# Optimization experiments

Hardware: AMD Instinct MI355X
Metric: run time of the kernel (lower is better)

The kernel has to match this reference:

```python
import jax, jax.numpy as jnp
import numpy as np

N_EMBD = 1024
N_HEAD = 16
B, T = 2, 2048
EPS_LN = 1e-5
EPS_RENORM = 1e-8


def _layernorm(x, w, b):
    mu = jnp.mean(x, axis=-1, keepdims=True)
    var = jnp.mean(jnp.square(x - mu), axis=-1, keepdims=True)
    return (x - mu) * jax.lax.rsqrt(var + EPS_LN) * w + b


def setup_inputs() -> dict:
    key = jax.random.key(0)
    ks = jax.random.split(key, 8)
    C = N_EMBD
    s = 0.02
    return {
        "x": jax.random.normal(ks[0], (B, T, C), jnp.float32),
        "ln1_w": jnp.ones((C,), jnp.float32),
        "ln1_b": jnp.zeros((C,), jnp.float32),
        "w_attn": jax.random.normal(ks[1], (C, 3 * C), jnp.float32) * s,
        "b_attn": jnp.zeros((3 * C,), jnp.float32),
        "w_attn_proj": jax.random.normal(ks[2], (C, C), jnp.float32) * s,
        "b_attn_proj": jnp.zeros((C,), jnp.float32),
        "threshold": jnp.full((N_HEAD,), 0.01, jnp.float32),
        "leak": jnp.full((N_HEAD,), 2.0, jnp.float32),
        "steepness": jnp.full((N_HEAD,), 2.0, jnp.float32),
        "ln2_w": jnp.ones((C,), jnp.float32),
        "ln2_b": jnp.zeros((C,), jnp.float32),
        "w_fc": jax.random.normal(ks[3], (C, 4 * C), jnp.float32) * s,
        "b_fc": jnp.zeros((4 * C,), jnp.float32),
        "w_mlp_proj": jax.random.normal(ks[4], (4 * C, C), jnp.float32) * s,
        "b_mlp_proj": jnp.zeros((C,), jnp.float32),
    }


def _ember_block(x, ln1_w, ln1_b, w_attn, b_attn, w_attn_proj, b_attn_proj,
                 threshold, leak, steepness, ln2_w, ln2_b,
                 w_fc, b_fc, w_mlp_proj, b_mlp_proj):
    Bx, Tx, C = x.shape
    H = N_HEAD
    D = C // H

    h = _layernorm(x, ln1_w, ln1_b)
    qkv = h @ w_attn + b_attn                      # [B,T,3C]
    q, k, v = jnp.split(qkv, 3, axis=-1)
    q = q.reshape(Bx, Tx, H, D).transpose(0, 2, 1, 3)  # [B,H,T,D]
    k = k.reshape(Bx, Tx, H, D).transpose(0, 2, 1, 3)
    v = v.reshape(Bx, Tx, H, D).transpose(0, 2, 1, 3)

    att = jnp.einsum('bhqd,bhkd->bhqk', q, k) * (1.0 / np.sqrt(D))
    causal = jnp.tril(jnp.ones((Tx, Tx), bool))
    att = jnp.where(causal[None, None], att, -jnp.inf)
    p = jax.nn.softmax(att, axis=-1)               # [B,H,T,T]

    # per-head LIF gating
    th = (jnp.abs(threshold) * 0.1)[None, :, None, None]
    lk = jax.nn.sigmoid(leak)[None, :, None, None]
    st = jax.nn.softplus(steepness)[None, :, None, None]
    fire = jax.nn.sigmoid(st * (p - th))
    w = fire + lk * (1.0 - fire)
    m = p * w
    m = m / (jnp.sum(m, axis=-1, keepdims=True) + EPS_RENORM)

    y = jnp.einsum('bhqk,bhkd->bhqd', m, v)
    y = y.transpose(0, 2, 1, 3).reshape(Bx, Tx, C)
    y = y @ w_attn_proj + b_attn_proj
    x = x + y

    h2 = _layernorm(x, ln2_w, ln2_b)
    h2 = jax.nn.gelu(h2 @ w_fc + b_fc, approximate=False)
    x = x + (h2 @ w_mlp_proj + b_mlp_proj)
    return x


def reference(x, ln1_w, ln1_b, w_attn, b_attn, w_attn_proj, b_attn_proj,
              threshold, leak, steepness, ln2_w, ln2_b,
              w_fc, b_fc, w_mlp_proj, b_mlp_proj):
    return _ember_block(x, ln1_w, ln1_b, w_attn, b_attn, w_attn_proj, b_attn_proj,
                        threshold, leak, steepness, ln2_w, ln2_b,
                        w_fc, b_fc, w_mlp_proj, b_mlp_proj)
```

## Files before the change

### kernel.cpp

```cpp
#include <hip/hip_runtime.h>
#include <hip/hip_bf16.h>
#include <math.h>

typedef __bf16 bf16_t;
typedef __bf16 bf16x8 __attribute__((ext_vector_type(8)));
typedef __bf16 bf16x4 __attribute__((ext_vector_type(4)));
typedef float  f32x4  __attribute__((ext_vector_type(4)));
typedef unsigned int u32;

static constexpr int C_    = 1024;
static constexpr int NH    = 16;
static constexpr int DH    = 64;
static constexpr int BB    = 2;
static constexpr int TT    = 2048;
static constexpr int MROWS = BB * TT;
static constexpr float LOG2E = 1.4426950408889634f;

__device__ __forceinline__ void gload_lds16(const bf16_t* src, bf16_t* dst) {
  __builtin_amdgcn_global_load_lds(
      (const __attribute__((address_space(1))) u32*)(src),
      (__attribute__((address_space(3))) u32*)(dst),
      16, 0, 0);
}

__device__ __forceinline__ u32 cvt_pk_bf16(float a, float b) {
  u32 r;
  asm("v_cvt_pk_bf16_f32 %0, %1, %2" : "=v"(r) : "v"(a), "v"(b));
  return r;
}

__device__ __forceinline__ float fexp2(float x) {
#if __has_builtin(__builtin_amdgcn_exp2f)
  return __builtin_amdgcn_exp2f(x);
#else
  return exp2f(x);
#endif
}
__device__ __forceinline__ float frcp(float x) {
#if __has_builtin(__builtin_amdgcn_rcpf)
  return __builtin_amdgcn_rcpf(x);
#else
  return 1.0f / x;
#endif
}

__device__ __forceinline__ int sc_to_t(int s, int c) {
  if (s < 32)  return s;
  if (s < 64)  return 32 + (s - 32) * 2 + c;
  if (s < 96)  return 96 + (s - 64) * 3 + c;
  return 192 + (s - 96) * 4 + c;
}

__device__ __forceinline__ void item64_to_uc(int item, int& u, int& c) {
  if (item < 8)       { u = item;               c = 0; }
  else if (item < 24) { int v = item - 8;  u = 8  + (v >> 1); c = v & 1; }
  else if (item < 48) { int v = item - 24; u = 16 + v / 3;    c = v - 3 * (v / 3); }
  else                { int v = item - 48; u = 24 + (v >> 2); c = v & 3; }
}

__global__ __launch_bounds__(256) void ln_bf16(
    const float* __restrict__ x, const float* __restrict__ w,
    const float* __restrict__ b, bf16_t* __restrict__ out)
{
  const int row = blockIdx.x;
  const int tid = threadIdx.x;
  const float4 v = reinterpret_cast<const float4*>(x + (size_t)row * C_)[tid];
  float s  = v.x + v.y + v.z + v.w;
  float s2 = v.x*v.x + v.y*v.y + v.z*v.z + v.w*v.w;
#pragma unroll
  for (int m = 1; m < 64; m <<= 1) { s += __shfl_xor(s, m); s2 += __shfl_xor(s2, m); }
  __shared__ float red[8];
  const int wv = tid >> 6;
  if ((tid & 63) == 0) { red[wv] = s; red[4 + wv] = s2; }
  __syncthreads();
  s  = red[0] + red[1] + red[2] + red[3];
  s2 = red[4] + red[5] + red[6] + red[7];
  const float mu   = s * (1.0f / C_);
  const float rstd = rsqrtf(s2 * (1.0f / C_) - mu * mu + 1e-5f);
  const float4 wv4 = reinterpret_cast<const float4*>(w)[tid];
  const float4 bv4 = reinterpret_cast<const float4*>(b)[tid];
  bf16x4 o;
  o[0] = (bf16_t)((v.x - mu) * rstd * wv4.x + bv4.x);
  o[1] = (bf16_t)((v.y - mu) * rstd * wv4.y + bv4.y);
  o[2] = (bf16_t)((v.z - mu) * rstd * wv4.z + bv4.z);
  o[3] = (bf16_t)((v.w - mu) * rstd * wv4.w + bv4.w);
  *reinterpret_cast<bf16x4*>(out + (size_t)row * C_ + tid * 4) = o;
}

__global__ __launch_bounds__(256) void ln2_fuse(
    const float* __restrict__ p0, const bf16_t* __restrict__ p1,
    const float* __restrict__ xin, const float* __restrict__ pbias,
    const float* __restrict__ w, const float* __restrict__ b,
    float* __restrict__ x2out, bf16_t* __restrict__ out)
{
  const int row = blockIdx.x;
  const int tid = threadIdx.x;
  const size_t base = (size_t)row * C_ + tid * 4;
  const float4 v0 = *reinterpret_cast<const float4*>(p0 + base);
  const bf16x4 v1 = *reinterpret_cast<const bf16x4*>(p1 + base);
  const float4 xr = *reinterpret_cast<const float4*>(xin + base);
  const float4 pb = *reinterpret_cast<const float4*>(pbias + tid * 4);
  float4 v;
  v.x = v0.x + (float)v1[0] + pb.x + xr.x;
  v.y = v0.y + (float)v1[1] + pb.y + xr.y;
  v.z = v0.z + (float)v1[2] + pb.z + xr.z;
  v.w = v0.w + (float)v1[3] + pb.w + xr.w;
  *reinterpret_cast<float4*>(x2out + base) = v;

  float s  = v.x + v.y + v.z + v.w;
  float s2 = v.x*v.x + v.y*v.y + v.z*v.z + v.w*v.w;
#pragma unroll
  for (int m = 1; m < 64; m <<= 1) { s += __shfl_xor(s, m); s2 += __shfl_xor(s2, m); }
  __shared__ float red[8];
  const int wv = tid >> 6;
  if ((tid & 63) == 0) { red[wv] = s; red[4 + wv] = s2; }
  __syncthreads();
  s  = red[0] + red[1] + red[2] + red[3];
  s2 = red[4] + red[5] + red[6] + red[7];
  const float mu   = s * (1.0f / C_);
  const float rstd = rsqrtf(s2 * (1.0f / C_) - mu * mu + 1e-5f);
  const float4 wv4 = reinterpret_cast<const float4*>(w)[tid];
  const float4 bv4 = reinterpret_cast<const float4*>(b)[tid];
  bf16x4 o;
  o[0] = (bf16_t)((v.x - mu) * rstd * wv4.x + bv4.x);
  o[1] = (bf16_t)((v.y - mu) * rstd * wv4.y + bv4.y);
  o[2] = (bf16_t)((v.z - mu) * rstd * wv4.z + bv4.z);
  o[3] = (bf16_t)((v.w - mu) * rstd * wv4.w + bv4.w);
  *reinterpret_cast<bf16x4*>(out + base) = o;
}

__global__ __launch_bounds__(256) void combine3(
    float* __restrict__ out, const bf16_t* __restrict__ p1,
    const bf16_t* __restrict__ p2, const bf16_t* __restrict__ p3,
    const float* __restrict__ bias, const float* __restrict__ resid)
{
  const size_t idx = ((size_t)blockIdx.x * 256 + threadIdx.x) * 4;
  float4 o = *reinterpret_cast<const float4*>(out + idx);
  const bf16x4 a = *reinterpret_cast<const bf16x4*>(p1 + idx);
  const bf16x4 b = *reinterpret_cast<const bf16x4*>(p2 + idx);
  const bf16x4 c = *reinterpret_cast<const bf16x4*>(p3 + idx);
  const float4 r = *reinterpret_cast<const float4*>(resid + idx);
  const int col = (int)(idx & (C_ - 1));
  const float4 bv = *reinterpret_cast<const float4*>(bias + col);
  o.x += (float)a[0] + (float)b[0] + (float)c[0] + bv.x + r.x;
  o.y += (float)a[1] + (float)b[1] + (float)c[1] + bv.y + r.y;
  o.z += (float)a[2] + (float)b[2] + (float)c[2] + bv.z + r.z;
  o.w += (float)a[3] + (float)b[3] + (float)c[3] + bv.w + r.w;
  *reinterpret_cast<float4*>(out + idx) = o;
}

__global__ __launch_bounds__(256) void transpose_w(
    const float* __restrict__ in, bf16_t* __restrict__ out, int K, int N)
{
  __shared__ float tile[32][33];
  const int tx = threadIdx.x & 31, ty = threadIdx.x >> 5;
  const int n0 = blockIdx.x * 32, k0 = blockIdx.y * 32;
#pragma unroll
  for (int i = 0; i < 4; ++i)
    tile[ty + i * 8][tx] = in[(size_t)(k0 + ty + i * 8) * N + n0 + tx];
  __syncthreads();
#pragma unroll
  for (int i = 0; i < 4; ++i)
    out[(size_t)(n0 + ty + i * 8) * K + k0 + tx] = (bf16_t)tile[tx][ty + i * 8];
}

__global__ __launch_bounds__(256) void transpose_v(
    const bf16_t* __restrict__ in, bf16_t* __restrict__ out)
{
  __shared__ bf16_t tile[32][33];
  const int bh = blockIdx.z;
  const bf16_t* src = in  + (size_t)bh * TT * DH;
  bf16_t*       dst = out + (size_t)bh * TT * DH;
  const int tx = threadIdx.x & 31, ty = threadIdx.x >> 5;
  const int t0 = blockIdx.x * 32, d0 = blockIdx.y * 32;
#pragma unroll
  for (int i = 0; i < 4; ++i)
    tile[ty + i * 8][tx] = src[(size_t)(t0 + ty + i * 8) * DH + d0 + tx];
  __syncthreads();
#pragma unroll
  for (int i = 0; i < 4; ++i)
    dst[(size_t)(d0 + ty + i * 8) * TT + t0 + tx] = tile[tx][ty + i * 8];
}

template<int EPI>
__global__ __launch_bounds__(256) void gemm_bf16(
    const bf16_t* __restrict__ A, const bf16_t* __restrict__ Bt,
    const float* __restrict__ bias, const float* __restrict__ resid,
    float* __restrict__ fout, bf16_t* __restrict__ bout0,
    bf16_t* __restrict__ bout1, bf16_t* __restrict__ bout2,
    int M, int N, int Kc, int Kfull)
{
  constexpr int BM = 128, BN = 128, BK = 64;
  __shared__ bf16_t As[BM * BK];
  __shared__ bf16_t Bs[BN * BK];
  const int tid  = threadIdx.x;
  const int wave = tid >> 6, lane = tid & 63;
  const int r = lane & 15, g = lane >> 4;
  const int wm = wave >> 1, wn = wave & 1;
  const int bm = blockIdx.x, bn = blockIdx.y;
  const int z  = blockIdx.z;
  const int kstart = z * Kc;

  const bf16_t* Abase = A  + (size_t)bm * BM * Kfull;
  const bf16_t* Bbase = Bt + (size_t)bn * BN * Kfull;

  f32x4 acc[4][4] = {};

  for (int kt = kstart; kt < kstart + Kc; kt += BK) {
#pragma unroll
    for (int it = 0; it < 4; ++it) {
      const int c0 = it * 256 + wave * 64;
      const int idx = c0 + lane;
      const int rr = idx >> 3, cc = idx & 7;
      const int gs = cc ^ (rr & 7);
      gload_lds16(Abase + (size_t)rr * Kfull + kt + gs * 8, As + c0 * 8);
    }
#pragma unroll
    for (int it = 0; it < 4; ++it) {
      const int c0 = it * 256 + wave * 64;
      const int idx = c0 + lane;
      const int rr = idx >> 3, cc = idx & 7;
      const int gs = cc ^ (rr & 7);
      gload_lds16(Bbase + (size_t)rr * Kfull + kt + gs * 8, Bs + c0 * 8);
    }
    asm volatile("s_waitcnt vmcnt(0)" ::: "memory");
    __syncthreads();
#pragma unroll
    for (int s = 0; s < 2; ++s) {
      bf16x8 af[4], bfr[4];
#pragma unroll
      for (int mi = 0; mi < 4; ++mi) {
        const int rr = wm * 64 + mi * 16 + r;
        const int ch = (s * 4 + g) ^ (rr & 7);
        af[mi] = *reinterpret_cast<const bf16x8*>(&As[rr * BK + ch * 8]);
      }
#pragma unroll
      for (int ni = 0; ni < 4; ++ni) {
        const int rr = wn * 64 + ni * 16 + r;
        const int ch = (s * 4 + g) ^ (rr & 7);
        bfr[ni] = *reinterpret_cast<const bf16x8*>(&Bs[rr * BK + ch * 8]);
      }
#pragma unroll
      for (int mi = 0; mi < 4; ++mi)
#pragma unroll
        for (int ni = 0; ni < 4; ++ni)
          acc[mi][ni] = __builtin_amdgcn_mfma_f32_16x16x32_bf16(
              af[mi], bfr[ni], acc[mi][ni], 0, 0, 0);
    }
    __syncthreads();
  }

#pragma unroll
  for (int mi = 0; mi < 4; ++mi) {
#pragma unroll
    for (int ni = 0; ni < 4; ++ni) {
      const int grow0 = bm * BM + wm * 64 + mi * 16 + g * 4;
      const int gcol  = bn * BN + wn * 64 + ni * 16 + r;
      const float bv = (EPI == 3) ? 0.f : bias[gcol];
#pragma unroll
      for (int i = 0; i < 4; ++i) {
        const int grow = grow0 + i;
        float v = acc[mi][ni][i] + bv;
        if constexpr (EPI == 0) {
          const int which = gcol >> 10;
          const int c0 = gcol & 1023;
          const int hh = c0 >> 6, dd = c0 & 63;
          const int bb = grow >> 11, t = grow & 2047;
          bf16_t* dst = (which == 0) ? bout0 : (which == 1) ? bout1 : bout2;
          dst[((size_t)(bb * NH + hh) * TT + t) * DH + dd] = (bf16_t)v;
        } else if constexpr (EPI == 1) {
          const size_t o = (size_t)grow * N + gcol;
          fout[o] = v + resid[o];
        } else if constexpr (EPI == 2) {
          const float gl = 0.5f * v * (1.0f + erff(v * 0.70710678118654752f));
          bout0[(size_t)grow * N + gcol] = (bf16_t)gl;
        } else {
          const size_t o = (size_t)grow * N + gcol;
          if (z == 0) fout[o] = v;
          else {
            bf16_t* pb = (z == 1) ? bout0 : (z == 2) ? bout1 : bout2;
            pb[o] = (bf16_t)v;
          }
        }
      }
    }
  }
}


__global__ __launch_bounds__(256, 4) void attn_p1(
    const bf16_t* __restrict__ Q, const bf16_t* __restrict__ Km,
    float2* __restrict__ mzP)
{
  __shared__ bf16_t Ks[2][64 * 64];
  const int tid = threadIdx.x;
  const int w = tid >> 6, lane = tid & 63;
  const int r = lane & 15, g = lane >> 4;
  const int bid = blockIdx.x;
  const int bh  = (bid & 7) * 4 + ((bid >> 3) & 3);
  int u, c; item64_to_uc(bid >> 5, u, c);
  const int cmax = u >> 3;
  const bool diag = (c == cmax);
  const int nt = diag ? (u & 7) + 1 : 8;
  const int s = 4 * u + w;
  const int row0 = u * 64 + w * 16;
  const int qrow = row0 + r;

  const bf16_t* Qh = Q  + (size_t)bh * TT * DH;
  const bf16_t* Kh = Km + (size_t)bh * TT * DH;
  const float SCL = 0.125f * LOG2E;

  bf16x8 qf[2];
#pragma unroll
  for (int s2 = 0; s2 < 2; ++s2) {
    bf16x8 t = *reinterpret_cast<const bf16x8*>(Qh + (size_t)qrow * DH + s2 * 32 + g * 8);
#pragma unroll
    for (int i = 0; i < 8; ++i) t[i] = (bf16_t)((float)t[i] * SCL);
    qf[s2] = t;
  }

  auto STAGEK = [&](int b, int t8) {
#pragma unroll
    for (int it = 0; it < 2; ++it) {
      const int idx = it * 256 + tid;
      const int rr = idx >> 3, cc = idx & 7, gs = cc ^ (rr & 7);
      gload_lds16(Kh + (size_t)(c * 512 + t8 * 64 + rr) * DH + gs * 8, &Ks[b][idx * 8]);
    }
  };

  float runM = -1e30f, runZ = 0.f;
  STAGEK(0, 0);
  for (int t8 = 0; t8 < nt; ++t8) {
    const int b = t8 & 1;
    asm volatile("s_waitcnt vmcnt(0)" ::: "memory");
    __syncthreads();
    if (t8 + 1 < nt) STAGEK(b ^ 1, t8 + 1);
    f32x4 sfT[4] = {};
#pragma unroll
    for (int s2 = 0; s2 < 2; ++s2) {
      bf16x8 kf[4];
#pragma unroll
      for (int ni = 0; ni < 4; ++ni)
        kf[ni] = *reinterpret_cast<const bf16x8*>(
            &Ks[b][(ni * 16 + r) * 64 + (((s2 << 2) | g) ^ (r & 7)) * 8]);
#pragma unroll
      for (int ni = 0; ni < 4; ++ni)
        sfT[ni] = __builtin_amdgcn_mfma_f32_16x16x32_bf16(kf[ni], qf[s2], sfT[ni], 0, 0, 0);
    }
    const bool dm = diag && (t8 == nt - 1);
    const int kbase = c * 512 + t8 * 64;
    float xv[16];
#pragma unroll
    for (int ni = 0; ni < 4; ++ni)
#pragma unroll
      for (int j = 0; j < 4; ++j) {
        float x = sfT[ni][j];
        if (dm) {
          const int kcol = kbase + ni * 16 + g * 4 + j;
          if (kcol > qrow) x = -1e30f;
        }
        xv[ni * 4 + j] = x;
      }
    float nm = runM;
#pragma unroll
    for (int e = 0; e < 16; ++e) nm = fmaxf(nm, xv[e]);
    float z = runZ * fexp2(runM - nm);
#pragma unroll
    for (int e = 0; e < 16; ++e) z += fexp2(xv[e] - nm);
    runM = nm; runZ = z;
  }
#pragma unroll
  for (int msk = 16; msk < 64; msk <<= 1) {
    const float om = __shfl_xor(runM, msk), oz = __shfl_xor(runZ, msk);
    const float nm = fmaxf(runM, om);
    runZ = runZ * fexp2(runM - nm) + oz * fexp2(om - nm);
    runM = nm;
  }
  if (lane < 16)
    mzP[((size_t)(bh * 128 + s) * 4 + c) * 16 + r] = make_float2(runM, runZ);
}

__global__ __launch_bounds__(256, 4) void attn_p3(
    const bf16_t* __restrict__ Q, const bf16_t* __restrict__ Km,
    const bf16_t* __restrict__ Vt, const float2* __restrict__ mzP,
    bf16_t* __restrict__ Y, uint2* __restrict__ yaccA,
    uint2* __restrict__ yaccB, float* __restrict__ denP,
    const float* __restrict__ thrp, const float* __restrict__ leakp,
    const float* __restrict__ steepp)
{
  __shared__ bf16_t Ks[2][64 * 64];
  __shared__ bf16_t Vs[2][64 * 64];
  __shared__ __align__(16) u32 Ms[4][512];

  const int tid = threadIdx.x;
  const int w = tid >> 6, lane = tid & 63;
  const int r = lane & 15, g = lane >> 4;
  const int bid = blockIdx.x;
  const int bh  = (bid & 7) * 4 + ((bid >> 3) & 3);
  int u, c; item64_to_uc(bid >> 5, u, c);
  const int cmax = u >> 3;
  const bool diag = (c == cmax);
  const int nt = diag ? (u & 7) + 1 : 8;
  const int nch = cmax + 1;
  const int s = 4 * u + w;
  const int row0 = u * 64 + w * 16;
  const int qrow = row0 + r;
  const int hh = bh & (NH - 1), bb = bh >> 4;

  const bf16_t* Qh  = Q  + (size_t)bh * TT * DH;
  const bf16_t* Kh  = Km + (size_t)bh * TT * DH;
  const bf16_t* Vth = Vt + (size_t)bh * TT * DH;

  const float lk  = 1.0f / (1.0f + expf(-leakp[hh]));
  const float ilk = 1.0f - lk;
  const float st  = log1pf(expf(steepp[hh]));
  const float Lst = LOG2E * st;
  const float A0  = Lst * (fabsf(thrp[hh]) * 0.1f);

  float M = -1e30f, Z = 0.f;
  for (int c2 = 0; c2 < nch; ++c2) {
    const float2 mz = mzP[((size_t)(bh * 128 + s) * 4 + c2) * 16 + r];
    const float nm = fmaxf(M, mz.x);
    Z = Z * fexp2(M - nm) + mz.y * fexp2(mz.x - nm);
    M = nm;
  }
  const float rcpZ = frcp(Z);

  const float SCL = 0.125f * LOG2E;
  bf16x8 qf[2];
#pragma unroll
  for (int s2 = 0; s2 < 2; ++s2) {
    bf16x8 t = *reinterpret_cast<const bf16x8*>(Qh + (size_t)qrow * DH + s2 * 32 + g * 8);
#pragma unroll
    for (int i = 0; i < 8; ++i) t[i] = (bf16_t)((float)t[i] * SCL);
    qf[s2] = t;
  }
  bf16x8 ones;
#pragma unroll
  for (int i = 0; i < 8; ++i) ones[i] = (bf16_t)1.0f;

  uint2* MsU2 = reinterpret_cast<uint2*>(&Ms[w][0]);
  uint4* MsU4 = reinterpret_cast<uint4*>(&Ms[w][0]);

  auto STAGE = [&](int b, int t8) {
    const int kbase = c * 512 + t8 * 64;
#pragma unroll
    for (int it = 0; it < 2; ++it) {
      const int idx = it * 256 + tid;
      const int rr = idx >> 3, cc = idx & 7, gs = cc ^ (rr & 7);
      gload_lds16(Kh + (size_t)(kbase + rr) * DH + gs * 8, &Ks[b][idx * 8]);
      gload_lds16(Vth + (size_t)rr * TT + kbase + gs * 8, &Vs[b][idx * 8]);
    }
  };

  f32x4 yacc[4] = {};
  f32x4 dacc = {};

  STAGE(0, 0);
  for (int t8 = 0; t8 < nt; ++t8) {
    const int b = t8 & 1;
    asm volatile("s_waitcnt vmcnt(0)" ::: "memory");
    __syncthreads();
    if (t8 + 1 < nt) STAGE(b ^ 1, t8 + 1);
    const int kbase = c * 512 + t8 * 64;
    f32x4 sfT[4] = {};
#pragma unroll
    for (int s2 = 0; s2 < 2; ++s2) {
      bf16x8 kf[4];
#pragma unroll
      for (int ni = 0; ni < 4; ++ni)
        kf[ni] = *reinterpret_cast<const bf16x8*>(
            &Ks[b][(ni * 16 + r) * 64 + (((s2 << 2) | g) ^ (r & 7)) * 8]);
#pragma unroll
      for (int ni = 0; ni < 4; ++ni)
        sfT[ni] = __builtin_amdgcn_mfma_f32_16x16x32_bf16(kf[ni], qf[s2], sfT[ni], 0, 0, 0);
    }
    const bool dm = diag && (t8 == nt - 1);
#pragma unroll
    for (int ni = 0; ni < 4; ++ni) {
      float mv[4];
#pragma unroll
      for (int j = 0; j < 4; ++j) {
        float x = sfT[ni][j];
        if (dm) {
          const int kcol = kbase + ni * 16 + g * 4 + j;
          if (kcol > qrow) x = -1e30f;
        }
        const float p    = fexp2(x - M) * rcpZ;
        const float fire = frcp(1.0f + fexp2(A0 - Lst * p));
        mv[j] = p * fmaf(ilk, fire, lk);
      }
      MsU2[r * 16 + ((4 * ni + g) ^ ((r & 7) << 1))] =
          make_uint2(cvt_pk_bf16(mv[0], mv[1]), cvt_pk_bf16(mv[2], mv[3]));
    }
#pragma unroll
    for (int s2 = 0; s2 < 2; ++s2) {
      const uint4 aw = MsU4[r * 8 + ((s2 * 4 + g) ^ (r & 7))];
      const bf16x8 af = __builtin_bit_cast(bf16x8, aw);
      bf16x8 vf[4];
#pragma unroll
      for (int ni = 0; ni < 4; ++ni)
        vf[ni] = *reinterpret_cast<const bf16x8*>(
            &Vs[b][(ni * 16 + r) * 64 + (((s2 << 2) | g) ^ (r & 7)) * 8]);
#pragma unroll
      for (int ni = 0; ni < 4; ++ni)
        yacc[ni] = __builtin_amdgcn_mfma_f32_16x16x32_bf16(af, vf[ni], yacc[ni], 0, 0, 0);
      dacc = __builtin_amdgcn_mfma_f32_16x16x32_bf16(af, ones, dacc, 0, 0, 0);
    }
  }

  if (nch == 1) {
#pragma unroll
    for (int j = 0; j < 4; ++j) {
      const float rd = frcp(dacc[j] + 1e-8f);
      const int t = row0 + g * 4 + j;
#pragma unroll
      for (int ni = 0; ni < 4; ++ni)
        Y[((size_t)(bb * TT + t)) * C_ + hh * DH + ni * 16 + r] =
            (bf16_t)(yacc[ni][j] * rd);
    }
  } else {
    const int pid = bh * 288 + (sc_to_t(s, c) - 32);
    uint2* pb = (pid < 4096) ? (yaccA + (size_t)pid * 256)
                             : (yaccB + (size_t)(pid - 4096) * 256);
#pragma unroll
    for (int ni = 0; ni < 4; ++ni)
      pb[ni * 64 + lane] =
          make_uint2(cvt_pk_bf16(yacc[ni][0], yacc[ni][1]),
                     cvt_pk_bf16(yacc[ni][2], yacc[ni][3]));
    if (r == 0)
      *reinterpret_cast<float4*>(&denP[(size_t)pid * 16 + g * 4]) =
          make_float4(dacc[0], dacc[1], dacc[2], dacc[3]);
  }
}

__global__ __launch_bounds__(256) void attn_p4(
    const uint2* __restrict__ yaccA, const uint2* __restrict__ yaccB,
    const float* __restrict__ denP, bf16_t* __restrict__ Y)
{
  const int bid = blockIdx.x;
  const int bh  = bid / 96;
  const int s   = 32 + (bid - bh * 96);
  const int nch = (s >> 5) + 1;
  const int hh = bh & (NH - 1), bb = bh >> 4;

  const int tid = threadIdx.x;
  const int w = tid >> 6, lane = tid & 63;
  const int r = lane & 15, g = lane >> 4;

  float acc[4] = {};
  float den[4] = {};
  for (int c = 0; c < nch; ++c) {
    const int pid = bh * 288 + (sc_to_t(s, c) - 32);
    const uint2* pb = (pid < 4096) ? (yaccA + (size_t)pid * 256)
                                   : (yaccB + (size_t)(pid - 4096) * 256);
    const uint2 u = pb[w * 64 + lane];
    acc[0] += __builtin_bit_cast(float, (u.x & 0xFFFFu) << 16);
    acc[1] += __builtin_bit_cast(float, (u.x & 0xFFFF0000u));
    acc[2] += __builtin_bit_cast(float, (u.y & 0xFFFFu) << 16);
    acc[3] += __builtin_bit_cast(float, (u.y & 0xFFFF0000u));
    const float4 d4 = *reinterpret_cast<const float4*>(&denP[(size_t)pid * 16 + g * 4]);
    den[0] += d4.x; den[1] += d4.y; den[2] += d4.z; den[3] += d4.w;
  }
#pragma unroll
  for (int j = 0; j < 4; ++j) {
    const float rd = 1.0f / (den[j] + 1e-8f);
    const int t = s * 16 + g * 4 + j;
    Y[((size_t)(bb * TT + t)) * C_ + hh * DH + w * 16 + r] = (bf16_t)(acc[j] * rd);
  }
}

extern "C" void kernel_launch(void* const* d_in, const int* in_sizes, int n_in,
                              void* d_out, int out_size, void* d_ws, size_t ws_size,
                              hipStream_t stream)
{
  const float* x      = (const float*)d_in[0];
  const float* ln1_w  = (const float*)d_in[1];
  const float* ln1_b  = (const float*)d_in[2];
  const float* w_attn = (const float*)d_in[3];
  const float* b_attn = (const float*)d_in[4];
  const float* w_proj = (const float*)d_in[5];
  const float* b_proj = (const float*)d_in[6];
  const float* thr    = (const float*)d_in[7];
  const float* leak   = (const float*)d_in[8];
  const float* steep  = (const float*)d_in[9];
  const float* ln2_w  = (const float*)d_in[10];
  const float* ln2_b  = (const float*)d_in[11];
  const float* w_fc   = (const float*)d_in[12];
  const float* b_fc   = (const float*)d_in[13];
  const float* w_mlp  = (const float*)d_in[14];
  const float* b_mlp  = (const float*)d_in[15];

  char* ws = (char*)d_ws;
  bf16_t* q    = (bf16_t*)(ws + 0);
  bf16_t* k    = (bf16_t*)(ws + 8388608);
  bf16_t* v    = (bf16_t*)(ws + 16777216);
  bf16_t* vT   = (bf16_t*)(ws + 25165824);
  bf16_t* gbuf = (bf16_t*)(ws + 0);
  bf16_t* hbuf = (bf16_t*)(ws + 33554432);
  float*  x2   = (float*) (ws + 41943040);
  bf16_t* wT_attn = (bf16_t*)(ws + 58720256);
  bf16_t* wT_proj = (bf16_t*)(ws + 65011712);
  bf16_t* wT_fc   = (bf16_t*)(ws + 67108864);
  bf16_t* wT_mlp  = (bf16_t*)(ws + 75497472);

  uint2* yaccA = (uint2*)(ws + 16777216);
  uint2* yaccB = (uint2*)(ws + 41943040);
  float* denP  = (float*)(ws + 52428800);
  float2* mzP  = (float2*)(ws + 53477376);

  bf16_t* pp1 = (bf16_t*)(ws + 0);
  bf16_t* mp1 = (bf16_t*)(ws + 33554432);
  bf16_t* mp2 = (bf16_t*)(ws + 58720256);
  bf16_t* mp3 = (bf16_t*)(ws + 67108864);

  float* out = (float*)d_out;

  ln_bf16<<<dim3(MROWS), dim3(256), 0, stream>>>(x, ln1_w, ln1_b, hbuf);
  transpose_w<<<dim3(96, 32),  dim3(256), 0, stream>>>(w_attn, wT_attn, 1024, 3072);
  transpose_w<<<dim3(32, 32),  dim3(256), 0, stream>>>(w_proj, wT_proj, 1024, 1024);
  transpose_w<<<dim3(128, 32), dim3(256), 0, stream>>>(w_fc,   wT_fc,   1024, 4096);
  transpose_w<<<dim3(32, 128), dim3(256), 0, stream>>>(w_mlp,  wT_mlp,  4096, 1024);

  gemm_bf16<0><<<dim3(32, 24, 1), dim3(256), 0, stream>>>(
      hbuf, wT_attn, b_attn, nullptr, nullptr, q, k, v, MROWS, 3072, 1024, 1024);
  transpose_v<<<dim3(64, 2, 32), dim3(256), 0, stream>>>(v, vT);

  attn_p1<<<dim3(2560), dim3(256), 0, stream>>>(q, k, mzP);
  attn_p3<<<dim3(2560), dim3(256), 0, stream>>>(
      q, k, vT, mzP, hbuf, yaccA, yaccB, denP, thr, leak, steep);
  attn_p4<<<dim3(3072), dim3(256), 0, stream>>>(yaccA, yaccB, denP, hbuf);

  gemm_bf16<3><<<dim3(32, 8, 2), dim3(256), 0, stream>>>(
      hbuf, wT_proj, nullptr, nullptr, x2, pp1, nullptr, nullptr,
      MROWS, 1024, 512, 1024);

  ln2_fuse<<<dim3(MROWS), dim3(256), 0, stream>>>(
      x2, pp1, x, b_proj, ln2_w, ln2_b, x2, hbuf);

  gemm_bf16<2><<<dim3(32, 32, 1), dim3(256), 0, stream>>>(
      hbuf, wT_fc, b_fc, nullptr, nullptr, gbuf, nullptr, nullptr,
      MROWS, 4096, 1024, 1024);

  gemm_bf16<3><<<dim3(32, 8, 4), dim3(256), 0, stream>>>(
      gbuf, wT_mlp, nullptr, nullptr, out, mp1, mp2, mp3,
      MROWS, 1024, 1024, 4096);

  combine3<<<dim3(4096), dim3(256), 0, stream>>>(out, mp1, mp2, mp3, b_mlp, x2);
}
```

Baseline: 295.2 us.

## Add double-buffered 256x256 tile GEMM for QKV and FC projections

Introduces a new GEMM kernel with 256x256 output tiles, 512 threads, XOR-swizzled LDS, double-buffered async global-to-LDS loads, grid swizzling and MFMA priority hints. It is used for the QKV projection and the FC+GELU GEMM. The old generic GEMM keeps only its split-K epilogue. Larger tiles raise arithmetic intensity and let loads overlap compute, but they launch far fewer blocks (192 and 256) on a chip with many CUs, which risks under-occupancy.

```diff
diff --git a/kernel.cpp b/kernel.cpp
--- a/kernel.cpp
+++ b/kernel.cpp
@@ -183,6 +183,106 @@
 }
 
 template<int EPI>
+__global__ __launch_bounds__(512, 2) void gemm256(
+    const bf16_t* __restrict__ A, const bf16_t* __restrict__ Bt,
+    const float* __restrict__ bias, bf16_t* __restrict__ bout0,
+    bf16_t* __restrict__ bout1, bf16_t* __restrict__ bout2,
+    int N, int K, int nbn)
+{
+  __shared__ bf16_t As[2][256 * 64];
+  __shared__ bf16_t Bs[2][256 * 64];
+  const int tid  = threadIdx.x;
+  const int wave = tid >> 6, lane = tid & 63;
+  const int r = lane & 15, g = lane >> 4;
+  const int wm = wave >> 2, wn = wave & 3;
+
+  const int cpx = gridDim.x >> 3;
+  const int swz = (blockIdx.x & 7) * cpx + (blockIdx.x >> 3);
+  const int bm = swz / nbn, bn = swz - bm * nbn;
+
+  const bf16_t* Abase = A  + (size_t)bm * 256 * K;
+  const bf16_t* Bbase = Bt + (size_t)bn * 256 * K;
+
+  f32x4 acc[8][4] = {};
+
+  auto STAGE = [&](int b, int kt) {
+#pragma unroll
+    for (int it = 0; it < 4; ++it) {
+      const int idx = it * 512 + tid;
+      const int rr = idx >> 3, cc = idx & 7, gs = cc ^ (rr & 7);
+      gload_lds16(Abase + (size_t)rr * K + kt + gs * 8, &As[b][idx * 8]);
+      gload_lds16(Bbase + (size_t)rr * K + kt + gs * 8, &Bs[b][idx * 8]);
+    }
+  };
+
+  const int NT = K >> 6;
+  STAGE(0, 0);
+  for (int t = 0; t < NT; ++t) {
+    const int b = t & 1;
+    if (t + 1 < NT) {
+      STAGE(b ^ 1, (t + 1) << 6);
+      asm volatile("s_waitcnt vmcnt(8)" ::: "memory");
+    } else {
+      asm volatile("s_waitcnt vmcnt(0)" ::: "memory");
+    }
+    __builtin_amdgcn_s_barrier();
+    asm volatile("" ::: "memory");
+#pragma unroll
+    for (int s2 = 0; s2 < 2; ++s2) {
+      bf16x8 af[8], bfr[4];
+#pragma unroll
+      for (int mi = 0; mi < 8; ++mi) {
+        const int rr = wm * 128 + mi * 16 + r;
+        const int ch = (s2 * 4 + g) ^ (rr & 7);
+        af[mi] = *reinterpret_cast<const bf16x8*>(&As[b][rr * 64 + ch * 8]);
+      }
+#pragma unroll
+      for (int ni = 0; ni < 4; ++ni) {
+        const int rr = wn * 64 + ni * 16 + r;
+        const int ch = (s2 * 4 + g) ^ (rr & 7);
+        bfr[ni] = *reinterpret_cast<const bf16x8*>(&Bs[b][rr * 64 + ch * 8]);
+      }
+      __builtin_amdgcn_s_setprio(1);
+#pragma unroll
+      for (int mi = 0; mi < 8; ++mi)
+#pragma unroll
+        for (int ni = 0; ni < 4; ++ni)
+          acc[mi][ni] = __builtin_amdgcn_mfma_f32_16x16x32_bf16(
+              af[mi], bfr[ni], acc[mi][ni], 0, 0, 0);
+      __builtin_amdgcn_s_setprio(0);
+    }
+    asm volatile("" ::: "memory");
+    __builtin_amdgcn_s_barrier();
+  }
+
+#pragma unroll
+  for (int mi = 0; mi < 8; ++mi) {
+#pragma unroll
+    for (int ni = 0; ni < 4; ++ni) {
+      const int grow0 = bm * 256 + wm * 128 + mi * 16 + g * 4;
+      const int gcol  = bn * 256 + wn * 64 + ni * 16 + r;
+      const float bv = bias[gcol];
+#pragma unroll
+      for (int i = 0; i < 4; ++i) {
+        const int grow = grow0 + i;
+        const float v = acc[mi][ni][i] + bv;
+        if constexpr (EPI == 0) {
+          const int which = gcol >> 10;
+          const int c0 = gcol & 1023;
+          const int hh = c0 >> 6, dd = c0 & 63;
+          const int bb = grow >> 11, tt = grow & 2047;
+          bf16_t* dst = (which == 0) ? bout0 : (which == 1) ? bout1 : bout2;
+          dst[((size_t)(bb * NH + hh) * TT + tt) * DH + dd] = (bf16_t)v;
+        } else {
+          const float gl = 0.5f * v * (1.0f + erff(v * 0.70710678118654752f));
+          bout0[(size_t)grow * N + gcol] = (bf16_t)gl;
+        }
+      }
+    }
+  }
+}
+
+template<int EPI>
 __global__ __launch_bounds__(256) void gemm_bf16(
     const bf16_t* __restrict__ A, const bf16_t* __restrict__ Bt,
     const float* __restrict__ bias, const float* __restrict__ resid,
@@ -256,31 +356,15 @@
     for (int ni = 0; ni < 4; ++ni) {
       const int grow0 = bm * BM + wm * 64 + mi * 16 + g * 4;
       const int gcol  = bn * BN + wn * 64 + ni * 16 + r;
-      const float bv = (EPI == 3) ? 0.f : bias[gcol];
 #pragma unroll
       for (int i = 0; i < 4; ++i) {
         const int grow = grow0 + i;
-        float v = acc[mi][ni][i] + bv;
-        if constexpr (EPI == 0) {
-          const int which = gcol >> 10;
-          const int c0 = gcol & 1023;
-          const int hh = c0 >> 6, dd = c0 & 63;
-          const int bb = grow >> 11, t = grow & 2047;
-          bf16_t* dst = (which == 0) ? bout0 : (which == 1) ? bout1 : bout2;
-          dst[((size_t)(bb * NH + hh) * TT + t) * DH + dd] = (bf16_t)v;
-        } else if constexpr (EPI == 1) {
-          const size_t o = (size_t)grow * N + gcol;
-          fout[o] = v + resid[o];
-        } else if constexpr (EPI == 2) {
-          const float gl = 0.5f * v * (1.0f + erff(v * 0.70710678118654752f));
-          bout0[(size_t)grow * N + gcol] = (bf16_t)gl;
-        } else {
-          const size_t o = (size_t)grow * N + gcol;
-          if (z == 0) fout[o] = v;
-          else {
-            bf16_t* pb = (z == 1) ? bout0 : (z == 2) ? bout1 : bout2;
-            pb[o] = (bf16_t)v;
-          }
+        const float v = acc[mi][ni][i];
+        const size_t o = (size_t)grow * N + gcol;
+        if (z == 0) fout[o] = v;
+        else {
+          bf16_t* pb = (z == 1) ? bout0 : (z == 2) ? bout1 : bout2;
+          pb[o] = (bf16_t)v;
         }
       }
     }
@@ -622,8 +706,8 @@
   transpose_w<<<dim3(128, 32), dim3(256), 0, stream>>>(w_fc,   wT_fc,   1024, 4096);
   transpose_w<<<dim3(32, 128), dim3(256), 0, stream>>>(w_mlp,  wT_mlp,  4096, 1024);
 
-  gemm_bf16<0><<<dim3(32, 24, 1), dim3(256), 0, stream>>>(
-      hbuf, wT_attn, b_attn, nullptr, nullptr, q, k, v, MROWS, 3072, 1024, 1024);
+  gemm256<0><<<dim3(192), dim3(512), 0, stream>>>(
+      hbuf, wT_attn, b_attn, q, k, v, 3072, 1024, 12);
   transpose_v<<<dim3(64, 2, 32), dim3(256), 0, stream>>>(v, vT);
 
   attn_p1<<<dim3(2560), dim3(256), 0, stream>>>(q, k, mzP);
@@ -638,9 +722,8 @@
   ln2_fuse<<<dim3(MROWS), dim3(256), 0, stream>>>(
       x2, pp1, x, b_proj, ln2_w, ln2_b, x2, hbuf);
 
-  gemm_bf16<2><<<dim3(32, 32, 1), dim3(256), 0, stream>>>(
-      hbuf, wT_fc, b_fc, nullptr, nullptr, gbuf, nullptr, nullptr,
-      MROWS, 4096, 1024, 1024);
+  gemm256<2><<<dim3(256), dim3(512), 0, stream>>>(
+      hbuf, wT_fc, b_fc, gbuf, nullptr, nullptr, 4096, 1024, 16);
 
   gemm_bf16<3><<<dim3(32, 8, 4), dim3(256), 0, stream>>>(
       gbuf, wT_mlp, nullptr, nullptr, out, mp1, mp2, mp3,
```

Result: no change. 295.5 us (+0.1%).

## Rewrite GEMM as 256x128 tile, 8-wave, triple-buffered pipelined kernel with grid swizzle

Applied to the files above, without the earlier changes.

Replaces the single-buffered 128x128 GEMM with a 512-thread kernel that computes 256x128 tiles and keeps three LDS stages in flight. Loads for tile t+2 are issued between MFMA groups, with partial vmcnt waits and raised wave priority around the MFMAs. A 1D grid is swizzled in groups of 8 to improve L2 reuse. The larger tiles and 144KB of LDS limit occupancy to one block per CU, and there are fewer blocks than before, which risks load imbalance on smaller GEMMs.

```diff
diff --git a/kernel.cpp b/kernel.cpp
--- a/kernel.cpp
+++ b/kernel.cpp
@@ -183,94 +183,116 @@
 }
 
 template<int EPI>
-__global__ __launch_bounds__(256) void gemm_bf16(
+__global__ __launch_bounds__(512, 1) void gemmP(
     const bf16_t* __restrict__ A, const bf16_t* __restrict__ Bt,
-    const float* __restrict__ bias, const float* __restrict__ resid,
-    float* __restrict__ fout, bf16_t* __restrict__ bout0,
-    bf16_t* __restrict__ bout1, bf16_t* __restrict__ bout2,
-    int M, int N, int Kc, int Kfull)
-{
-  constexpr int BM = 128, BN = 128, BK = 64;
-  __shared__ bf16_t As[BM * BK];
-  __shared__ bf16_t Bs[BN * BK];
+    const float* __restrict__ bias, float* __restrict__ fout,
+    bf16_t* __restrict__ bout0, bf16_t* __restrict__ bout1,
+    bf16_t* __restrict__ bout2, int N, int Kc, int Kfull, int nbn)
+{
+  __shared__ bf16_t As[3][256 * 64];
+  __shared__ bf16_t Bs[3][128 * 64];
   const int tid  = threadIdx.x;
   const int wave = tid >> 6, lane = tid & 63;
   const int r = lane & 15, g = lane >> 4;
-  const int wm = wave >> 1, wn = wave & 1;
-  const int bm = blockIdx.x, bn = blockIdx.y;
+  const int wm = wave >> 2, wn = wave & 3;
+
+  const int cpx = gridDim.x >> 3;
+  const int swz = (blockIdx.x & 7) * cpx + (blockIdx.x >> 3);
+  const int bm = swz / nbn, bn = swz - bm * nbn;
   const int z  = blockIdx.z;
-  const int kstart = z * Kc;
-
-  const bf16_t* Abase = A  + (size_t)bm * BM * Kfull;
-  const bf16_t* Bbase = Bt + (size_t)bn * BN * Kfull;
-
-  f32x4 acc[4][4] = {};
-
-  for (int kt = kstart; kt < kstart + Kc; kt += BK) {
-#pragma unroll
-    for (int it = 0; it < 4; ++it) {
-      const int c0 = it * 256 + wave * 64;
-      const int idx = c0 + lane;
-      const int rr = idx >> 3, cc = idx & 7;
-      const int gs = cc ^ (rr & 7);
-      gload_lds16(Abase + (size_t)rr * Kfull + kt + gs * 8, As + c0 * 8);
-    }
-#pragma unroll
-    for (int it = 0; it < 4; ++it) {
-      const int c0 = it * 256 + wave * 64;
-      const int idx = c0 + lane;
-      const int rr = idx >> 3, cc = idx & 7;
-      const int gs = cc ^ (rr & 7);
-      gload_lds16(Bbase + (size_t)rr * Kfull + kt + gs * 8, Bs + c0 * 8);
-    }
-    asm volatile("s_waitcnt vmcnt(0)" ::: "memory");
-    __syncthreads();
-#pragma unroll
-    for (int s = 0; s < 2; ++s) {
-      bf16x8 af[4], bfr[4];
-#pragma unroll
-      for (int mi = 0; mi < 4; ++mi) {
-        const int rr = wm * 64 + mi * 16 + r;
-        const int ch = (s * 4 + g) ^ (rr & 7);
-        af[mi] = *reinterpret_cast<const bf16x8*>(&As[rr * BK + ch * 8]);
+  const int k0 = z * Kc;
+
+  const bf16_t* Abase = A  + (size_t)bm * 256 * Kfull + k0;
+  const bf16_t* Bbase = Bt + (size_t)bn * 128 * Kfull + k0;
+
+  f32x4 acc[8][2] = {};
+
+  auto STAGE_A = [&](int buf, int kt, int pass) {
+    const int idx = pass * 512 + tid;
+    const int rr = idx >> 3, cc = idx & 7, gs = cc ^ (rr & 7);
+    gload_lds16(Abase + (size_t)rr * Kfull + kt + gs * 8, &As[buf][idx * 8]);
+  };
+  auto STAGE_B = [&](int buf, int kt, int pass) {
+    const int idx = pass * 512 + tid;
+    const int rr = idx >> 3, cc = idx & 7, gs = cc ^ (rr & 7);
+    gload_lds16(Bbase + (size_t)rr * Kfull + kt + gs * 8, &Bs[buf][idx * 8]);
+  };
+  auto STAGE6 = [&](int buf, int kt) {
+    STAGE_A(buf, kt, 0); STAGE_A(buf, kt, 1);
+    STAGE_A(buf, kt, 2); STAGE_A(buf, kt, 3);
+    STAGE_B(buf, kt, 0); STAGE_B(buf, kt, 1);
+  };
+
+  const int NT = Kc >> 6;
+  STAGE6(0, 0);
+  STAGE6(1, 64);
+
+  for (int t = 0; t < NT; ++t) {
+    const int buf = t % 3;
+    if (t + 1 < NT) asm volatile("s_waitcnt vmcnt(6)" ::: "memory");
+    else            asm volatile("s_waitcnt vmcnt(0)" ::: "memory");
+    __builtin_amdgcn_s_barrier();
+    asm volatile("" ::: "memory");
+
+    const bool pre = (t + 2 < NT);
+    const int kn   = (t + 2) << 6;
+    const int bnx  = (t + 2) % 3;
+
+    bf16x8 bfr[2][2];
+#pragma unroll
+    for (int s2 = 0; s2 < 2; ++s2)
+#pragma unroll
+      for (int ni = 0; ni < 2; ++ni) {
+        const int rr = wn * 32 + ni * 16 + r;
+        bfr[s2][ni] = *reinterpret_cast<const bf16x8*>(
+            &Bs[buf][rr * 64 + (((s2 << 2) | g) ^ (rr & 7)) * 8]);
       }
 #pragma unroll
-      for (int ni = 0; ni < 4; ++ni) {
-        const int rr = wn * 64 + ni * 16 + r;
-        const int ch = (s * 4 + g) ^ (rr & 7);
-        bfr[ni] = *reinterpret_cast<const bf16x8*>(&Bs[rr * BK + ch * 8]);
+    for (int mh = 0; mh < 2; ++mh) {
+      bf16x8 af[2][4];
+#pragma unroll
+      for (int s2 = 0; s2 < 2; ++s2)
+#pragma unroll
+        for (int mi = 0; mi < 4; ++mi) {
+          const int rr = wm * 128 + (mh * 4 + mi) * 16 + r;
+          af[s2][mi] = *reinterpret_cast<const bf16x8*>(
+              &As[buf][rr * 64 + (((s2 << 2) | g) ^ (rr & 7)) * 8]);
+        }
+      if (pre) {
+        if (mh == 0) { STAGE_A(bnx, kn, 0); STAGE_A(bnx, kn, 1); STAGE_A(bnx, kn, 2); }
+        else         { STAGE_A(bnx, kn, 3); STAGE_B(bnx, kn, 0); STAGE_B(bnx, kn, 1); }
       }
-#pragma unroll
-      for (int mi = 0; mi < 4; ++mi)
-#pragma unroll
-        for (int ni = 0; ni < 4; ++ni)
-          acc[mi][ni] = __builtin_amdgcn_mfma_f32_16x16x32_bf16(
-              af[mi], bfr[ni], acc[mi][ni], 0, 0, 0);
-    }
-    __syncthreads();
-  }
-
-#pragma unroll
-  for (int mi = 0; mi < 4; ++mi) {
-#pragma unroll
-    for (int ni = 0; ni < 4; ++ni) {
-      const int grow0 = bm * BM + wm * 64 + mi * 16 + g * 4;
-      const int gcol  = bn * BN + wn * 64 + ni * 16 + r;
+      __builtin_amdgcn_s_setprio(1);
+#pragma unroll
+      for (int s2 = 0; s2 < 2; ++s2)
+#pragma unroll
+        for (int mi = 0; mi < 4; ++mi)
+#pragma unroll
+          for (int ni = 0; ni < 2; ++ni)
+            acc[mh * 4 + mi][ni] = __builtin_amdgcn_mfma_f32_16x16x32_bf16(
+                af[s2][mi], bfr[s2][ni], acc[mh * 4 + mi][ni], 0, 0, 0);
+      __builtin_amdgcn_s_setprio(0);
+    }
+  }
+
+#pragma unroll
+  for (int mi = 0; mi < 8; ++mi) {
+#pragma unroll
+    for (int ni = 0; ni < 2; ++ni) {
+      const int grow0 = bm * 256 + wm * 128 + mi * 16 + g * 4;
+      const int gcol  = bn * 128 + wn * 32 + ni * 16 + r;
       const float bv = (EPI == 3) ? 0.f : bias[gcol];
 #pragma unroll
       for (int i = 0; i < 4; ++i) {
         const int grow = grow0 + i;
-        float v = acc[mi][ni][i] + bv;
+        const float v = acc[mi][ni][i] + bv;
         if constexpr (EPI == 0) {
           const int which = gcol >> 10;
           const int c0 = gcol & 1023;
           const int hh = c0 >> 6, dd = c0 & 63;
-          const int bb = grow >> 11, t = grow & 2047;
+          const int bb = grow >> 11, tt = grow & 2047;
           bf16_t* dst = (which == 0) ? bout0 : (which == 1) ? bout1 : bout2;
-          dst[((size_t)(bb * NH + hh) * TT + t) * DH + dd] = (bf16_t)v;
-        } else if constexpr (EPI == 1) {
-          const size_t o = (size_t)grow * N + gcol;
-          fout[o] = v + resid[o];
+          dst[((size_t)(bb * NH + hh) * TT + tt) * DH + dd] = (bf16_t)v;
         } else if constexpr (EPI == 2) {
           const float gl = 0.5f * v * (1.0f + erff(v * 0.70710678118654752f));
           bout0[(size_t)grow * N + gcol] = (bf16_t)gl;
@@ -622,8 +644,8 @@
   transpose_w<<<dim3(128, 32), dim3(256), 0, stream>>>(w_fc,   wT_fc,   1024, 4096);
   transpose_w<<<dim3(32, 128), dim3(256), 0, stream>>>(w_mlp,  wT_mlp,  4096, 1024);
 
-  gemm_bf16<0><<<dim3(32, 24, 1), dim3(256), 0, stream>>>(
-      hbuf, wT_attn, b_attn, nullptr, nullptr, q, k, v, MROWS, 3072, 1024, 1024);
+  gemmP<0><<<dim3(384, 1, 1), dim3(512), 0, stream>>>(
+      hbuf, wT_attn, b_attn, nullptr, q, k, v, 3072, 1024, 1024, 24);
   transpose_v<<<dim3(64, 2, 32), dim3(256), 0, stream>>>(v, vT);
 
   attn_p1<<<dim3(2560), dim3(256), 0, stream>>>(q, k, mzP);
@@ -631,20 +653,17 @@
       q, k, vT, mzP, hbuf, yaccA, yaccB, denP, thr, leak, steep);
   attn_p4<<<dim3(3072), dim3(256), 0, stream>>>(yaccA, yaccB, denP, hbuf);
 
-  gemm_bf16<3><<<dim3(32, 8, 2), dim3(256), 0, stream>>>(
-      hbuf, wT_proj, nullptr, nullptr, x2, pp1, nullptr, nullptr,
-      MROWS, 1024, 512, 1024);
+  gemmP<3><<<dim3(128, 1, 2), dim3(512), 0, stream>>>(
+      hbuf, wT_proj, nullptr, x2, pp1, nullptr, nullptr, 1024, 512, 1024, 8);
 
   ln2_fuse<<<dim3(MROWS), dim3(256), 0, stream>>>(
       x2, pp1, x, b_proj, ln2_w, ln2_b, x2, hbuf);
 
-  gemm_bf16<2><<<dim3(32, 32, 1), dim3(256), 0, stream>>>(
-      hbuf, wT_fc, b_fc, nullptr, nullptr, gbuf, nullptr, nullptr,
-      MROWS, 4096, 1024, 1024);
-
-  gemm_bf16<3><<<dim3(32, 8, 4), dim3(256), 0, stream>>>(
-      gbuf, wT_mlp, nullptr, nullptr, out, mp1, mp2, mp3,
-      MROWS, 1024, 1024, 4096);
+  gemmP<2><<<dim3(512, 1, 1), dim3(512), 0, stream>>>(
+      hbuf, wT_fc, b_fc, nullptr, gbuf, nullptr, nullptr, 4096, 1024, 1024, 32);
+
+  gemmP<3><<<dim3(128, 1, 4), dim3(512), 0, stream>>>(
+      gbuf, wT_mlp, nullptr, out, mp1, mp2, mp3, 1024, 1024, 4096, 8);
 
   combine3<<<dim3(4096), dim3(256), 0, stream>>>(out, mp1, mp2, mp3, b_mlp, x2);
 }
```

After: 292.9 us. No clear change (-0.8%).
